# Optimization experiments

Hardware: AMD Instinct MI355X
Metric: run time of the kernel (lower is better)

The kernel has to match this reference:

```python
import jax, jax.numpy as jnp
import numpy as np

K_POW = 3.0
EPS = 1e-6

def _weight1(d, r):
    # (1 - (d/r)^2)^k for d < r else 0; guard base before float power
    base = jnp.where(d < r, 1.0 - (d / r) ** 2, 0.0)
    return base ** K_POW

def _weight2(d, r):
    # 1 for d < r/2; (1 - ((2d-r)/r)^2)^k for r/2 <= d < r; else 0
    band = (d >= r / 2) & (d < r)
    base = jnp.where(band, 1.0 - ((2.0 * d - r) / r) ** 2, 0.0)
    return jnp.where(d < r / 2, 1.0, base ** K_POW)

def setup_inputs() -> dict:
    key = jax.random.key(0)
    ks = jax.random.split(key, 10)
    n, p, L = 4096, 128, 32
    x = jax.random.uniform(ks[0], (n, p), dtype=jnp.float32)
    s = 0.05
    return {
        "x": x,
        "r0": jnp.float32(4.0),
        "r1": jnp.float32(2.0),
        "r2": jnp.float32(4.0),
        "We1": jax.random.normal(ks[1], (L, p), jnp.float32) * s,
        "be1": jnp.zeros((L,), jnp.float32),
        "We2": jax.random.normal(ks[2], (L, L), jnp.float32) * s,
        "be2": jnp.zeros((L,), jnp.float32),
        "Wd1": jax.random.normal(ks[3], (L, L), jnp.float32) * s,
        "bd1": jnp.zeros((L,), jnp.float32),
        "Wd2": jax.random.normal(ks[4], (p, L), jnp.float32) * s,
        "bd2": jnp.zeros((p,), jnp.float32),
    }

def _mr_layer(x, r0, r1, r2):
    y = x  # y = x.clone()
    x2 = jnp.sum(x * x, axis=-1)
    d2 = x2[:, None] + x2[None, :] - 2.0 * (x @ x.T)  # (n, n)
    dist = jnp.sqrt(jnp.maximum(d2, 1e-12))
    md = dist.max()
    # torch reassigns r to max_dist when r > max_dist -> min(r, max_dist)
    r0e = jnp.minimum(r0, md)
    r1e = jnp.minimum(r1, md)
    r2e = jnp.minimum(r2, md)
    # inds = any(dist <= r0) is all-true (diag is ~0), so no row selection needed
    alpha = _weight1(dist, r0e)
    alpha = alpha / jnp.sum(alpha, axis=0, keepdims=True)
    mu = alpha.T @ x  # (n, p)
    mu = jnp.where(jnp.isnan(mu), y, mu)
    U = y - mu  # (n, p); contraction direction per point
    # projection scalar ps[i,j] = <x_i - y_j, U_j>, avoiding (n,n,p) diff tensor
    ps = x @ U.T - jnp.sum(y * U, axis=-1)[None, :]  # (n, n)
    u_norm2 = jnp.sum(U * U, axis=-1)[None, :]  # (1, n)
    dist_u2 = jnp.maximum(ps ** 2 * u_norm2, EPS)
    dist_v = jnp.sqrt(jnp.maximum(dist ** 2 - dist_u2, EPS))
    dist_u = jnp.sqrt(dist_u2)
    beta = _weight2(dist_v, r1e) * _weight2(dist_u, r2e)
    beta = beta / jnp.sum(beta, axis=0, keepdims=True)
    e_Z = beta.T @ x
    e_Z = jnp.where(jnp.isnan(e_Z), y, e_Z)
    return e_Z

def reference(x, r0, r1, r2, We1, be1, We2, be2, Wd1, bd1, Wd2, bd2):
    y = _mr_layer(x, r0, r1, r2)
    # encoder: Linear -> GELU(exact) -> Linear
    h = jax.nn.gelu(y @ We1.T + be1, approximate=False)
    z = h @ We2.T + be2
    # decoder: Linear -> GELU(exact) -> Linear -> Sigmoid
    h2 = jax.nn.gelu(z @ Wd1.T + bd1, approximate=False)
    x_hat = jax.nn.sigmoid(h2 @ Wd2.T + bd2)
    # loss = lam_recon * MSE(x, x_hat); lam_topo = lam_geom = 0
    return jnp.mean((x - x_hat) ** 2)
```

## Files before the change

kernel.cpp:

```cpp
#include <hip/hip_runtime.h>
#include <math.h>

#define N 4096
#define P 128
#define LDIM 32
#define CHUNKS 8
#define ITILES 4

typedef unsigned int u32;
typedef unsigned short u16;
typedef short s16x8 __attribute__((ext_vector_type(8)));
typedef float f32x4 __attribute__((ext_vector_type(4)));

__device__ __forceinline__ u16 f2b(float f) {
  u32 u = __float_as_uint(f);
  u += 0x7fffu + ((u >> 16) & 1u);
  return (u16)(u >> 16);
}
__device__ __forceinline__ float b2f(u16 h) { return __uint_as_float(((u32)h) << 16); }

__device__ __forceinline__ float w2f(float d, float r) {
  if (d < 0.5f * r) return 1.0f;
  if (d < r) { float t = (2.0f * d - r) / r; float b = 1.0f - t * t; return b * b * b; }
  return 0.0f;
}
__device__ __forceinline__ float geluf(float a) {
  return 0.5f * a * (1.0f + erff(a * 0.70710678118654752f));
}

#define MFMA(a, b, c) __builtin_amdgcn_mfma_f32_16x16x32_bf16((a), (b), (c), 0, 0, 0)

__global__ void k_init(u32* __restrict__ mdb, float* __restrict__ out) {
  if (threadIdx.x == 0) { *mdb = 0u; out[0] = 0.0f; }
}

__global__ __launch_bounds__(256) void k_prep(const float* __restrict__ x, u16* __restrict__ xb,
                                              u16* __restrict__ xbT, float* __restrict__ x2) {
  __shared__ u16 tlT[128][40];
  const int bi = blockIdx.x * 32;
  const int tid = threadIdx.x;
  const int r = tid >> 3, cg = (tid & 7) * 16;
  const float* src = &x[(size_t)(bi + r) * P + cg];
  float4 v0 = *(const float4*)(src + 0);
  float4 v1 = *(const float4*)(src + 4);
  float4 v2 = *(const float4*)(src + 8);
  float4 v3 = *(const float4*)(src + 12);
  u16 h[16];
  h[0] = f2b(v0.x); h[1] = f2b(v0.y); h[2] = f2b(v0.z); h[3] = f2b(v0.w);
  h[4] = f2b(v1.x); h[5] = f2b(v1.y); h[6] = f2b(v1.z); h[7] = f2b(v1.w);
  h[8] = f2b(v2.x); h[9] = f2b(v2.y); h[10] = f2b(v2.z); h[11] = f2b(v2.w);
  h[12] = f2b(v3.x); h[13] = f2b(v3.y); h[14] = f2b(v3.z); h[15] = f2b(v3.w);
  float s = 0.0f;
#pragma unroll
  for (int e = 0; e < 16; e++) { float f = b2f(h[e]); s = fmaf(f, f, s); }
  s += __shfl_down(s, 4); s += __shfl_down(s, 2); s += __shfl_down(s, 1);
  if ((tid & 7) == 0) x2[bi + r] = s;
  uint4 p0, p1;
  p0.x = (u32)h[0] | ((u32)h[1] << 16);  p0.y = (u32)h[2] | ((u32)h[3] << 16);
  p0.z = (u32)h[4] | ((u32)h[5] << 16);  p0.w = (u32)h[6] | ((u32)h[7] << 16);
  p1.x = (u32)h[8] | ((u32)h[9] << 16);  p1.y = (u32)h[10] | ((u32)h[11] << 16);
  p1.z = (u32)h[12] | ((u32)h[13] << 16); p1.w = (u32)h[14] | ((u32)h[15] << 16);
  *(uint4*)&xb[(size_t)(bi + r) * P + cg] = p0;
  *(uint4*)&xb[(size_t)(bi + r) * P + cg + 8] = p1;
#pragma unroll
  for (int e = 0; e < 16; e++) tlT[cg + e][r] = h[e];
  __syncthreads();
  const int c = tid >> 1, hh = tid & 1;
  uint4 q0 = *(const uint4*)&tlT[c][hh * 16];
  uint4 q1 = *(const uint4*)&tlT[c][hh * 16 + 8];
  *(uint4*)&xbT[(size_t)c * N + bi + hh * 16] = q0;
  *(uint4*)&xbT[(size_t)c * N + bi + hh * 16 + 8] = q1;
}

__global__ __launch_bounds__(128) void k_anchor(const u16* __restrict__ xb, const float* __restrict__ x2,
                                                u32* __restrict__ mdb) {
  const int i = blockIdx.x * 128 + threadIdx.x;
  const uint4* ra = (const uint4*)(xb + (size_t)i * P);
  const uint4* r0 = (const uint4*)xb;
  float dot = 0.0f;
#pragma unroll
  for (int q = 0; q < 16; ++q) {
    uint4 a = ra[q], b = r0[q];
    u32 aa[4] = {a.x, a.y, a.z, a.w}, bb[4] = {b.x, b.y, b.z, b.w};
#pragma unroll
    for (int e = 0; e < 4; e++) {
      dot = fmaf(b2f((u16)(aa[e] & 0xffffu)), b2f((u16)(bb[e] & 0xffffu)), dot);
      dot = fmaf(b2f((u16)(aa[e] >> 16)), b2f((u16)(bb[e] >> 16)), dot);
    }
  }
  float d2 = fmaxf(x2[i] + x2[0] - 2.0f * dot, 0.0f);
#pragma unroll
  for (int o = 32; o > 0; o >>= 1) d2 = fmaxf(d2, __shfl_down(d2, o));
  if ((threadIdx.x & 63) == 0) atomicMax(mdb, __float_as_uint(d2));
}

__global__ __launch_bounds__(512, 4) void k_grammax(const u16* __restrict__ xb, const float* __restrict__ x2,
                                                    u32* __restrict__ mdb,
                                                    const float* __restrict__ r0p, const float* __restrict__ r1p,
                                                    const float* __restrict__ r2p) {
  const float rmax = fmaxf(r0p[0], fmaxf(r1p[0], r2p[0])) * 1.02f;
  if (__uint_as_float(*mdb) >= rmax * rmax) return;
  __shared__ uint4 LA[1024];
  const int j0 = blockIdx.x * 64;
  const int cid = blockIdx.y;
  if (cid * 512 + 512 <= j0) return;
  const int tid = threadIdx.x;
  const int lane = tid & 63, w = tid >> 6;
  const int lm = lane & 15, quad = lane >> 4;
  {
    const uint4* g = (const uint4*)(xb + (size_t)j0 * P);
#pragma unroll
    for (int it = 0; it < 2; ++it) {
      int c = it * 512 + tid;
      int row = c >> 4, ch = c & 15;
      LA[row * 16 + (ch ^ (row & 7))] = g[c];
    }
  }
  float x2j[4][4];
#pragma unroll
  for (int u = 0; u < 4; u++)
#pragma unroll
    for (int reg = 0; reg < 4; reg++) x2j[u][reg] = x2[j0 + u * 16 + quad * 4 + reg];
  __syncthreads();
  float lmax = 0.0f;
  for (int t = 0; t < ITILES; ++t) {
    const int i0 = cid * 512 + t * 128;
    if (i0 + 128 <= j0) continue;
    f32x4 accG[4];
#pragma unroll
    for (int u = 0; u < 4; u++) accG[u] = {0.f, 0.f, 0.f, 0.f};
    const u16* gb = xb + (size_t)(i0 + w * 16 + lm) * P;
#pragma unroll
    for (int ks = 0; ks < 4; ++ks) {
      s16x8 bf = *(const s16x8*)(gb + ks * 32 + quad * 8);
      s16x8 af[4];
#pragma unroll
      for (int u = 0; u < 4; u++) { int m = u * 16 + lm; af[u] = *(const s16x8*)&LA[m * 16 + ((ks * 4 + quad) ^ (m & 7))]; }
#pragma unroll
      for (int u = 0; u < 4; u++) accG[u] = MFMA(af[u], bf, accG[u]);
    }
    float x2i = x2[i0 + w * 16 + lm];
#pragma unroll
    for (int u = 0; u < 4; u++)
#pragma unroll
      for (int reg = 0; reg < 4; reg++) lmax = fmaxf(lmax, x2j[u][reg] + x2i - 2.0f * accG[u][reg]);
  }
#pragma unroll
  for (int o = 32; o > 0; o >>= 1) lmax = fmaxf(lmax, __shfl_down(lmax, o));
  if (lane == 0) atomicMax(mdb, __float_as_uint(lmax));
}

__global__ __launch_bounds__(512, 4) void k_alpha(const u16* __restrict__ xb, const u16* __restrict__ xbT,
                                                  const float* __restrict__ x2,
                                                  float* __restrict__ muP, float* __restrict__ S1P,
                                                  const float* __restrict__ r0p, const u32* __restrict__ mdb) {
  __shared__ uint4 LA[1024];
  __shared__ u16 W16[64 * 136];
  const int j0 = blockIdx.x * 64, cid = blockIdx.y;
  const int tid = threadIdx.x;
  const int lane = tid & 63, w = tid >> 6;
  const int lm = lane & 15, quad = lane >> 4;
  {
    const uint4* g = (const uint4*)(xb + (size_t)j0 * P);
#pragma unroll
    for (int it = 0; it < 2; ++it) {
      int c = it * 512 + tid;
      int row = c >> 4, ch = c & 15;
      LA[row * 16 + (ch ^ (row & 7))] = g[c];
    }
  }
  const float mdf = sqrtf(fmaxf(__uint_as_float(*mdb), 1e-12f));
  const float re = fminf(r0p[0], mdf);
  const float re2 = re * re, inv_re2 = 1.0f / re2;
  float x2j[4];
#pragma unroll
  for (int v = 0; v < 4; v++) x2j[v] = x2[j0 + v * 16 + lm];
  f32x4 accPV[4], accS[4];
#pragma unroll
  for (int u = 0; u < 4; u++) { accPV[u] = {0.f, 0.f, 0.f, 0.f}; accS[u] = {0.f, 0.f, 0.f, 0.f}; }
  const s16x8 ones = {0x3F80, 0x3F80, 0x3F80, 0x3F80, 0x3F80, 0x3F80, 0x3F80, 0x3F80};
  __syncthreads();
  for (int t = 0; t < ITILES; ++t) {
    const int i0 = cid * 512 + t * 128;
    f32x4 accG[4];
#pragma unroll
    for (int v = 0; v < 4; v++) accG[v] = {0.f, 0.f, 0.f, 0.f};
    const u16* ga = xb + (size_t)(i0 + w * 16 + lm) * P;
#pragma unroll
    for (int ks = 0; ks < 4; ++ks) {
      s16x8 af = *(const s16x8*)(ga + ks * 32 + quad * 8);
      s16x8 bf[4];
#pragma unroll
      for (int v = 0; v < 4; v++) { int m = v * 16 + lm; bf[v] = *(const s16x8*)&LA[m * 16 + ((ks * 4 + quad) ^ (m & 7))]; }
#pragma unroll
      for (int v = 0; v < 4; v++) accG[v] = MFMA(af, bf[v], accG[v]);
    }
    float4 x2iv = *(const float4*)&x2[i0 + w * 16 + quad * 4];
    const float xi[4] = {x2iv.x, x2iv.y, x2iv.z, x2iv.w};
    u16 wv4[4][4];
#pragma unroll
    for (int v = 0; v < 4; v++)
#pragma unroll
      for (int reg = 0; reg < 4; reg++) {
        float d2 = fmaxf(xi[reg] + x2j[v] - 2.0f * accG[v][reg], 1e-12f);
        float wt = 0.0f;
        if (d2 < re2) { float b = 1.0f - d2 * inv_re2; wt = b * b * b; }
        wv4[v][reg] = f2b(wt);
      }
    __syncthreads();
#pragma unroll
    for (int v = 0; v < 4; v++) {
      ushort4 pk; pk.x = wv4[v][0]; pk.y = wv4[v][1]; pk.z = wv4[v][2]; pk.w = wv4[v][3];
      *(ushort4*)&W16[(v * 16 + lm) * 136 + w * 16 + quad * 4] = pk;
    }
    __syncthreads();
    const u16* gx = xbT + (size_t)(w * 16 + lm) * N + i0;
#pragma unroll
    for (int ks = 0; ks < 4; ++ks) {
      s16x8 bx = *(const s16x8*)(gx + ks * 32 + quad * 8);
      s16x8 aw[4];
#pragma unroll
      for (int u = 0; u < 4; u++) { int m = u * 16 + lm; aw[u] = *(const s16x8*)&W16[m * 136 + ks * 32 + quad * 8]; }
#pragma unroll
      for (int u = 0; u < 4; u++) accPV[u] = MFMA(aw[u], bx, accPV[u]);
      if (w == 0) {
#pragma unroll
        for (int u = 0; u < 4; u++) accS[u] = MFMA(aw[u], ones, accS[u]);
      }
    }
  }
  float* mu = muP + (size_t)cid * N * P;
#pragma unroll
  for (int u = 0; u < 4; u++)
#pragma unroll
    for (int reg = 0; reg < 4; reg++)
      mu[(size_t)(j0 + u * 16 + quad * 4 + reg) * P + w * 16 + lm] = accPV[u][reg];
  if (w == 0 && lm == 0) {
#pragma unroll
    for (int u = 0; u < 4; u++)
#pragma unroll
      for (int reg = 0; reg < 4; reg++)
        S1P[cid * N + j0 + u * 16 + quad * 4 + reg] = accS[u][reg];
  }
}

__global__ __launch_bounds__(128) void k_finU(const float* __restrict__ x, const u16* __restrict__ xb,
                                              const float* __restrict__ muP, const float* __restrict__ S1P,
                                              u16* __restrict__ Ub, float* __restrict__ u2, float* __restrict__ cj) {
  const int j = blockIdx.x, t = threadIdx.x;
  float ssum = 0.0f, msum = 0.0f;
#pragma unroll
  for (int c = 0; c < CHUNKS; ++c) {
    ssum += S1P[c * N + j];
    msum += muP[((size_t)c * N + j) * P + t];
  }
  float xv = x[(size_t)j * P + t];
  float uval = 0.0f;
  if (ssum > 0.0f) uval = xv - msum / ssum;
  u16 ub = f2b(uval);
  Ub[(size_t)j * P + t] = ub;
  float uf = b2f(ub);
  float xbf = b2f(xb[(size_t)j * P + t]);
  float a = uf * uf, b = xbf * uf;
#pragma unroll
  for (int o = 32; o > 0; o >>= 1) { a += __shfl_down(a, o); b += __shfl_down(b, o); }
  __shared__ float ra[2], rb[2];
  if ((t & 63) == 0) { ra[t >> 6] = a; rb[t >> 6] = b; }
  __syncthreads();
  if (t == 0) { u2[j] = ra[0] + ra[1]; cj[j] = rb[0] + rb[1]; }
}

__global__ __launch_bounds__(512, 4) void k_betaez(const u16* __restrict__ xb, const u16* __restrict__ Ub,
                                                   const u16* __restrict__ xbT,
                                                   const float* __restrict__ x2, const float* __restrict__ u2,
                                                   const float* __restrict__ cj,
                                                   float* __restrict__ ezP, float* __restrict__ S2P,
                                                   const float* __restrict__ r1p, const float* __restrict__ r2p,
                                                   const u32* __restrict__ mdb) {
  __shared__ uint4 LA[1024];
  __shared__ uint4 LU[1024];
  __shared__ u16 W16[64 * 136];
  const int j0 = blockIdx.x * 64, cid = blockIdx.y;
  const int tid = threadIdx.x;
  const int lane = tid & 63, w = tid >> 6;
  const int lm = lane & 15, quad = lane >> 4;
  {
    const uint4* ga = (const uint4*)(xb + (size_t)j0 * P);
    const uint4* gu = (const uint4*)(Ub + (size_t)j0 * P);
#pragma unroll
    for (int it = 0; it < 2; ++it) {
      int c = it * 512 + tid;
      int row = c >> 4, ch = c & 15;
      int sw = row * 16 + (ch ^ (row & 7));
      LA[sw] = ga[c];
      LU[sw] = gu[c];
    }
  }
  const float mdf = sqrtf(fmaxf(__uint_as_float(*mdb), 1e-12f));
  const float r1e = fminf(r1p[0], mdf), r2e = fminf(r2p[0], mdf);
  float x2j[4], u2j[4], ncj[4];
#pragma unroll
  for (int v = 0; v < 4; v++) {
    int jj = j0 + v * 16 + lm;
    x2j[v] = x2[jj]; u2j[v] = u2[jj]; ncj[v] = -cj[jj];
  }
  f32x4 accPV[4], accS[4];
#pragma unroll
  for (int u = 0; u < 4; u++) { accPV[u] = {0.f, 0.f, 0.f, 0.f}; accS[u] = {0.f, 0.f, 0.f, 0.f}; }
  const s16x8 ones = {0x3F80, 0x3F80, 0x3F80, 0x3F80, 0x3F80, 0x3F80, 0x3F80, 0x3F80};
  __syncthreads();
  for (int t = 0; t < ITILES; ++t) {
    const int i0 = cid * 512 + t * 128;
    f32x4 accG[4], accP[4];
#pragma unroll
    for (int v = 0; v < 4; v++) {
      accG[v] = {0.f, 0.f, 0.f, 0.f};
      accP[v] = {ncj[v], ncj[v], ncj[v], ncj[v]};
    }
    const u16* ga = xb + (size_t)(i0 + w * 16 + lm) * P;
#pragma unroll
    for (int ks = 0; ks < 4; ++ks) {
      s16x8 af = *(const s16x8*)(ga + ks * 32 + quad * 8);
      s16x8 bf[4], bu[4];
#pragma unroll
      for (int v = 0; v < 4; v++) {
        int m = v * 16 + lm;
        int off = m * 16 + ((ks * 4 + quad) ^ (m & 7));
        bf[v] = *(const s16x8*)&LA[off];
        bu[v] = *(const s16x8*)&LU[off];
      }
#pragma unroll
      for (int v = 0; v < 4; v++) {
        accG[v] = MFMA(af, bf[v], accG[v]);
        accP[v] = MFMA(af, bu[v], accP[v]);
      }
    }
    float4 x2iv = *(const float4*)&x2[i0 + w * 16 + quad * 4];
    const float xi[4] = {x2iv.x, x2iv.y, x2iv.z, x2iv.w};
    u16 wv4[4][4];
#pragma unroll
    for (int v = 0; v < 4; v++)
#pragma unroll
      for (int reg = 0; reg < 4; reg++) {
        float d2 = fmaxf(xi[reg] + x2j[v] - 2.0f * accG[v][reg], 1e-12f);
        float ps = accP[v][reg];
        float du2 = fmaxf(ps * ps * u2j[v], 1e-6f);
        float dv = sqrtf(fmaxf(d2 - du2, 1e-6f));
        float du = sqrtf(du2);
        wv4[v][reg] = f2b(w2f(dv, r1e) * w2f(du, r2e));
      }
    __syncthreads();
#pragma unroll
    for (int v = 0; v < 4; v++) {
      ushort4 pk; pk.x = wv4[v][0]; pk.y = wv4[v][1]; pk.z = wv4[v][2]; pk.w = wv4[v][3];
      *(ushort4*)&W16[(v * 16 + lm) * 136 + w * 16 + quad * 4] = pk;
    }
    __syncthreads();
    const u16* gx = xbT + (size_t)(w * 16 + lm) * N + i0;
#pragma unroll
    for (int ks = 0; ks < 4; ++ks) {
      s16x8 bx = *(const s16x8*)(gx + ks * 32 + quad * 8);
      s16x8 aw[4];
#pragma unroll
      for (int u = 0; u < 4; u++) { int m = u * 16 + lm; aw[u] = *(const s16x8*)&W16[m * 136 + ks * 32 + quad * 8]; }
#pragma unroll
      for (int u = 0; u < 4; u++) accPV[u] = MFMA(aw[u], bx, accPV[u]);
      if (w == 0) {
#pragma unroll
        for (int u = 0; u < 4; u++) accS[u] = MFMA(aw[u], ones, accS[u]);
      }
    }
  }
  float* ez = ezP + (size_t)cid * N * P;
#pragma unroll
  for (int u = 0; u < 4; u++)
#pragma unroll
    for (int reg = 0; reg < 4; reg++)
      ez[(size_t)(j0 + u * 16 + quad * 4 + reg) * P + w * 16 + lm] = accPV[u][reg];
  if (w == 0 && lm == 0) {
#pragma unroll
    for (int u = 0; u < 4; u++)
#pragma unroll
      for (int reg = 0; reg < 4; reg++)
        S2P[cid * N + j0 + u * 16 + quad * 4 + reg] = accS[u][reg];
  }
}

#define AE_ROWS 16
__global__ __launch_bounds__(256) void k_ae(const float* __restrict__ x, const float* __restrict__ ezP,
                                            const float* __restrict__ S2P,
                                            const float* __restrict__ We1, const float* __restrict__ be1,
                                            const float* __restrict__ We2, const float* __restrict__ be2,
                                            const float* __restrict__ Wd1, const float* __restrict__ bd1,
                                            const float* __restrict__ Wd2, const float* __restrict__ bd2,
                                            float* __restrict__ out) {
  __shared__ float We1T[P][33];
  __shared__ float We2T[LDIM][33];
  __shared__ float Wd1T[LDIM][33];
  __shared__ float Wd2T[LDIM][129];
  __shared__ float ezs[AE_ROWS][P];
  __shared__ float h1s[AE_ROWS][LDIM], zbs[AE_ROWS][LDIM], h2s[AE_ROWS][LDIM];
  __shared__ float be1s[LDIM], be2s[LDIM], bd1s[LDIM], bd2s[P];
  __shared__ float s2s[AE_ROWS];
  const int tid = threadIdx.x;
  const int r0 = blockIdx.x * AE_ROWS;
  for (int idx = tid; idx < P * LDIM; idx += 256) {
    int o = idx >> 7, k = idx & 127;
    We1T[k][o] = We1[idx];
    int o2 = idx >> 5, k2 = idx & 31;
    Wd2T[k2][o2] = Wd2[idx];
  }
  for (int idx = tid; idx < LDIM * LDIM; idx += 256) {
    int o = idx >> 5, k = idx & 31;
    We2T[k][o] = We2[idx];
    Wd1T[k][o] = Wd1[idx];
  }
  if (tid < LDIM) { be1s[tid] = be1[tid]; be2s[tid] = be2[tid]; bd1s[tid] = bd1[tid]; }
  if (tid < P) bd2s[tid] = bd2[tid];
  if (tid < AE_ROWS) {
    float s = 0.0f;
#pragma unroll
    for (int c = 0; c < CHUNKS; ++c) s += S2P[c * N + r0 + tid];
    s2s[tid] = s;
  }
  __syncthreads();
  for (int idx = tid; idx < AE_ROWS * P; idx += 256) {
    int r = idx >> 7, col = idx & 127;
    int row = r0 + r;
    float es = 0.0f;
#pragma unroll
    for (int c = 0; c < CHUNKS; ++c) es += ezP[((size_t)c * N + row) * P + col];
    float xv = x[(size_t)row * P + col];
    ezs[r][col] = (s2s[r] > 0.0f) ? (es / s2s[r]) : xv;
  }
  __syncthreads();
  {
    const int o = tid & 31, rh = tid >> 5;
#pragma unroll
    for (int rr = 0; rr < 2; rr++) {
      int r = rh + rr * 8;
      float a = be1s[o];
#pragma unroll 8
      for (int k = 0; k < P; k++) a = fmaf(We1T[k][o], ezs[r][k], a);
      h1s[r][o] = geluf(a);
    }
  }
  __syncthreads();
  {
    const int o = tid & 31, rh = tid >> 5;
#pragma unroll
    for (int rr = 0; rr < 2; rr++) {
      int r = rh + rr * 8;
      float a = be2s[o];
#pragma unroll
      for (int k = 0; k < LDIM; k++) a = fmaf(We2T[k][o], h1s[r][k], a);
      zbs[r][o] = a;
    }
  }
  __syncthreads();
  {
    const int o = tid & 31, rh = tid >> 5;
#pragma unroll
    for (int rr = 0; rr < 2; rr++) {
      int r = rh + rr * 8;
      float a = bd1s[o];
#pragma unroll
      for (int k = 0; k < LDIM; k++) a = fmaf(Wd1T[k][o], zbs[r][k], a);
      h2s[r][o] = geluf(a);
    }
  }
  __syncthreads();
  {
    const int o = tid & 127, rh = tid >> 7;
    float part = 0.0f;
#pragma unroll
    for (int rr = 0; rr < 8; rr++) {
      int r = rh + rr * 2;
      int row = r0 + r;
      float a = bd2s[o];
#pragma unroll
      for (int k = 0; k < LDIM; k++) a = fmaf(Wd2T[k][o], h2s[r][k], a);
      float xh = 1.0f / (1.0f + expf(-a));
      float diff = x[(size_t)row * P + o] - xh;
      part = fmaf(diff, diff, part);
    }
#pragma unroll
    for (int off = 32; off > 0; off >>= 1) part += __shfl_down(part, off);
    if ((tid & 63) == 0) atomicAdd(out, part * (1.0f / ((float)N * (float)P)));
  }
}

extern "C" void kernel_launch(void* const* d_in, const int* in_sizes, int n_in,
                              void* d_out, int out_size, void* d_ws, size_t ws_size,
                              hipStream_t stream) {
  const float* x   = (const float*)d_in[0];
  const float* r0  = (const float*)d_in[1];
  const float* r1  = (const float*)d_in[2];
  const float* r2  = (const float*)d_in[3];
  const float* We1 = (const float*)d_in[4];
  const float* be1 = (const float*)d_in[5];
  const float* We2 = (const float*)d_in[6];
  const float* be2 = (const float*)d_in[7];
  const float* Wd1 = (const float*)d_in[8];
  const float* bd1 = (const float*)d_in[9];
  const float* Wd2 = (const float*)d_in[10];
  const float* bd2 = (const float*)d_in[11];
  float* out = (float*)d_out;

  char* base = (char*)d_ws;
  size_t off = 0;
  u16* xb  = (u16*)(base + off); off += (size_t)N * P * 2;
  u16* xbT = (u16*)(base + off); off += (size_t)N * P * 2;
  u16* Ub  = (u16*)(base + off); off += (size_t)N * P * 2;
  float* muP = (float*)(base + off); off += (size_t)CHUNKS * N * P * 4;
  float* ezP = (float*)(base + off); off += (size_t)CHUNKS * N * 4 * P / 4 * 4;
  float* S1P = (float*)(base + off); off += (size_t)CHUNKS * N * 4;
  float* S2P = (float*)(base + off); off += (size_t)CHUNKS * N * 4;
  float* x2  = (float*)(base + off); off += (size_t)N * 4;
  u32* mdb   = (u32*)(base + off); off += 4;
  float* u2  = (float*)(base + off); off += (size_t)N * 4;
  float* cjv = (float*)(base + off); off += (size_t)N * 4;

  hipLaunchKernelGGL(k_init, dim3(1), dim3(64), 0, stream, mdb, out);
  hipLaunchKernelGGL(k_prep, dim3(N / 32), dim3(256), 0, stream, x, xb, xbT, x2);
  hipLaunchKernelGGL(k_anchor, dim3(N / 128), dim3(128), 0, stream, xb, x2, mdb);
  hipLaunchKernelGGL(k_grammax, dim3(N / 64, CHUNKS), dim3(512), 0, stream, xb, x2, mdb, r0, r1, r2);
  hipLaunchKernelGGL(k_alpha, dim3(N / 64, CHUNKS), dim3(512), 0, stream, xb, xbT, x2, muP, S1P, r0, mdb);
  hipLaunchKernelGGL(k_finU, dim3(N), dim3(128), 0, stream, x, xb, muP, S1P, Ub, u2, cjv);
  hipLaunchKernelGGL(k_betaez, dim3(N / 64, CHUNKS), dim3(512), 0, stream, xb, Ub, xbT, x2, u2, cjv, ezP, S2P, r1, r2, mdb);
  hipLaunchKernelGGL(k_ae, dim3(N / AE_ROWS), dim3(256), 0, stream, x, ezP, S2P, We1, be1, We2, be2, Wd1, bd1, Wd2, bd2, out);
}
```

Baseline: 186.9 us.

## Split alpha/beta passes into more chunks, swizzle weight LDS, compute row sums in VALU

Raises the number of i-chunks in the alpha kernel from 8 to 16 and in the beta kernel from 8 to 12 (uneven 3/2 tile split), giving more blocks and higher launch-bound occupancy. The weight tile in LDS switches from a padded layout to an XOR-swizzled layout. The column-sum of weights is now accumulated in registers and reduced through shared-memory atomics, replacing the extra MFMA-against-ones done by wave 0. In exchange, partial buffers grow and the finalize and autoencoder kernels must read more chunks.

```diff
diff --git a/kernel.cpp b/kernel.cpp
--- a/kernel.cpp
+++ b/kernel.cpp
@@ -4,8 +4,8 @@
 #define N 4096
 #define P 128
 #define LDIM 32
-#define CHUNKS 8
-#define ITILES 4
+#define CHA 16
+#define CHB 12
 
 typedef unsigned int u32;
 typedef unsigned short u16;
@@ -123,7 +123,7 @@
     for (int reg = 0; reg < 4; reg++) x2j[u][reg] = x2[j0 + u * 16 + quad * 4 + reg];
   __syncthreads();
   float lmax = 0.0f;
-  for (int t = 0; t < ITILES; ++t) {
+  for (int t = 0; t < 4; ++t) {
     const int i0 = cid * 512 + t * 128;
     if (i0 + 128 <= j0) continue;
     f32x4 accG[4];
@@ -150,12 +150,14 @@
   if (lane == 0) atomicMax(mdb, __float_as_uint(lmax));
 }
 
-__global__ __launch_bounds__(512, 4) void k_alpha(const u16* __restrict__ xb, const u16* __restrict__ xbT,
+__global__ __launch_bounds__(512, 8) void k_alpha(const u16* __restrict__ xb, const u16* __restrict__ xbT,
                                                   const float* __restrict__ x2,
                                                   float* __restrict__ muP, float* __restrict__ S1P,
                                                   const float* __restrict__ r0p, const u32* __restrict__ mdb) {
   __shared__ uint4 LA[1024];
-  __shared__ u16 W16[64 * 136];
+  __shared__ uint4 WS[1024];
+  __shared__ float S1L[64];
+  u16* W16 = (u16*)WS;
   const int j0 = blockIdx.x * 64, cid = blockIdx.y;
   const int tid = threadIdx.x;
   const int lane = tid & 63, w = tid >> 6;
@@ -169,19 +171,21 @@
       LA[row * 16 + (ch ^ (row & 7))] = g[c];
     }
   }
+  if (tid < 64) S1L[tid] = 0.0f;
   const float mdf = sqrtf(fmaxf(__uint_as_float(*mdb), 1e-12f));
   const float re = fminf(r0p[0], mdf);
   const float re2 = re * re, inv_re2 = 1.0f / re2;
   float x2j[4];
 #pragma unroll
   for (int v = 0; v < 4; v++) x2j[v] = x2[j0 + v * 16 + lm];
-  f32x4 accPV[4], accS[4];
-#pragma unroll
-  for (int u = 0; u < 4; u++) { accPV[u] = {0.f, 0.f, 0.f, 0.f}; accS[u] = {0.f, 0.f, 0.f, 0.f}; }
-  const s16x8 ones = {0x3F80, 0x3F80, 0x3F80, 0x3F80, 0x3F80, 0x3F80, 0x3F80, 0x3F80};
-  __syncthreads();
-  for (int t = 0; t < ITILES; ++t) {
-    const int i0 = cid * 512 + t * 128;
+  f32x4 accPV[4];
+#pragma unroll
+  for (int u = 0; u < 4; u++) accPV[u] = {0.f, 0.f, 0.f, 0.f};
+  float sjv[4] = {0.f, 0.f, 0.f, 0.f};
+  __syncthreads();
+#pragma unroll
+  for (int t = 0; t < 2; ++t) {
+    const int i0 = (cid * 2 + t) * 128;
     f32x4 accG[4];
 #pragma unroll
     for (int v = 0; v < 4; v++) accG[v] = {0.f, 0.f, 0.f, 0.f};
@@ -205,13 +209,19 @@
         float d2 = fmaxf(xi[reg] + x2j[v] - 2.0f * accG[v][reg], 1e-12f);
         float wt = 0.0f;
         if (d2 < re2) { float b = 1.0f - d2 * inv_re2; wt = b * b * b; }
-        wv4[v][reg] = f2b(wt);
+        u16 hv = f2b(wt);
+        wv4[v][reg] = hv;
+        sjv[v] += b2f(hv);
       }
     __syncthreads();
-#pragma unroll
-    for (int v = 0; v < 4; v++) {
-      ushort4 pk; pk.x = wv4[v][0]; pk.y = wv4[v][1]; pk.z = wv4[v][2]; pk.w = wv4[v][3];
-      *(ushort4*)&W16[(v * 16 + lm) * 136 + w * 16 + quad * 4] = pk;
+    {
+      const int ch = 2 * w + (quad >> 1), sub = (quad & 1) * 4;
+#pragma unroll
+      for (int v = 0; v < 4; v++) {
+        int row = v * 16 + lm;
+        ushort4 pk; pk.x = wv4[v][0]; pk.y = wv4[v][1]; pk.z = wv4[v][2]; pk.w = wv4[v][3];
+        *(ushort4*)&W16[(row * 16 + (ch ^ (row & 7))) * 8 + sub] = pk;
+      }
     }
     __syncthreads();
     const u16* gx = xbT + (size_t)(w * 16 + lm) * N + i0;
@@ -220,13 +230,12 @@
       s16x8 bx = *(const s16x8*)(gx + ks * 32 + quad * 8);
       s16x8 aw[4];
 #pragma unroll
-      for (int u = 0; u < 4; u++) { int m = u * 16 + lm; aw[u] = *(const s16x8*)&W16[m * 136 + ks * 32 + quad * 8]; }
+      for (int u = 0; u < 4; u++) {
+        int m = u * 16 + lm;
+        aw[u] = *(const s16x8*)&W16[(m * 16 + ((ks * 4 + quad) ^ (m & 7))) * 8];
+      }
 #pragma unroll
       for (int u = 0; u < 4; u++) accPV[u] = MFMA(aw[u], bx, accPV[u]);
-      if (w == 0) {
-#pragma unroll
-        for (int u = 0; u < 4; u++) accS[u] = MFMA(aw[u], ones, accS[u]);
-      }
     }
   }
   float* mu = muP + (size_t)cid * N * P;
@@ -235,13 +244,10 @@
 #pragma unroll
     for (int reg = 0; reg < 4; reg++)
       mu[(size_t)(j0 + u * 16 + quad * 4 + reg) * P + w * 16 + lm] = accPV[u][reg];
-  if (w == 0 && lm == 0) {
-#pragma unroll
-    for (int u = 0; u < 4; u++)
-#pragma unroll
-      for (int reg = 0; reg < 4; reg++)
-        S1P[cid * N + j0 + u * 16 + quad * 4 + reg] = accS[u][reg];
-  }
+#pragma unroll
+  for (int v = 0; v < 4; v++) atomicAdd(&S1L[v * 16 + lm], sjv[v]);
+  __syncthreads();
+  if (tid < 64) S1P[cid * N + j0 + tid] = S1L[tid];
 }
 
 __global__ __launch_bounds__(128) void k_finU(const float* __restrict__ x, const u16* __restrict__ xb,
@@ -250,7 +256,7 @@
   const int j = blockIdx.x, t = threadIdx.x;
   float ssum = 0.0f, msum = 0.0f;
 #pragma unroll
-  for (int c = 0; c < CHUNKS; ++c) {
+  for (int c = 0; c < CHA; ++c) {
     ssum += S1P[c * N + j];
     msum += muP[((size_t)c * N + j) * P + t];
   }
@@ -270,7 +276,7 @@
   if (t == 0) { u2[j] = ra[0] + ra[1]; cj[j] = rb[0] + rb[1]; }
 }
 
-__global__ __launch_bounds__(512, 4) void k_betaez(const u16* __restrict__ xb, const u16* __restrict__ Ub,
+__global__ __launch_bounds__(512, 6) void k_betaez(const u16* __restrict__ xb, const u16* __restrict__ Ub,
                                                    const u16* __restrict__ xbT,
                                                    const float* __restrict__ x2, const float* __restrict__ u2,
                                                    const float* __restrict__ cj,
@@ -279,7 +285,9 @@
                                                    const u32* __restrict__ mdb) {
   __shared__ uint4 LA[1024];
   __shared__ uint4 LU[1024];
-  __shared__ u16 W16[64 * 136];
+  __shared__ uint4 WS[1024];
+  __shared__ float S2L[64];
+  u16* W16 = (u16*)WS;
   const int j0 = blockIdx.x * 64, cid = blockIdx.y;
   const int tid = threadIdx.x;
   const int lane = tid & 63, w = tid >> 6;
@@ -296,6 +304,7 @@
       LU[sw] = gu[c];
     }
   }
+  if (tid < 64) S2L[tid] = 0.0f;
   const float mdf = sqrtf(fmaxf(__uint_as_float(*mdb), 1e-12f));
   const float r1e = fminf(r1p[0], mdf), r2e = fminf(r2p[0], mdf);
   float x2j[4], u2j[4], ncj[4];
@@ -304,13 +313,15 @@
     int jj = j0 + v * 16 + lm;
     x2j[v] = x2[jj]; u2j[v] = u2[jj]; ncj[v] = -cj[jj];
   }
-  f32x4 accPV[4], accS[4];
-#pragma unroll
-  for (int u = 0; u < 4; u++) { accPV[u] = {0.f, 0.f, 0.f, 0.f}; accS[u] = {0.f, 0.f, 0.f, 0.f}; }
-  const s16x8 ones = {0x3F80, 0x3F80, 0x3F80, 0x3F80, 0x3F80, 0x3F80, 0x3F80, 0x3F80};
-  __syncthreads();
-  for (int t = 0; t < ITILES; ++t) {
-    const int i0 = cid * 512 + t * 128;
+  f32x4 accPV[4];
+#pragma unroll
+  for (int u = 0; u < 4; u++) accPV[u] = {0.f, 0.f, 0.f, 0.f};
+  float sjv[4] = {0.f, 0.f, 0.f, 0.f};
+  const int tstart = (cid < 8) ? cid * 3 : 24 + (cid - 8) * 2;
+  const int tcnt = (cid < 8) ? 3 : 2;
+  __syncthreads();
+  for (int t = 0; t < tcnt; ++t) {
+    const int i0 = (tstart + t) * 128;
     f32x4 accG[4], accP[4];
 #pragma unroll
     for (int v = 0; v < 4; v++) {
@@ -347,13 +358,19 @@
         float du2 = fmaxf(ps * ps * u2j[v], 1e-6f);
         float dv = sqrtf(fmaxf(d2 - du2, 1e-6f));
         float du = sqrtf(du2);
-        wv4[v][reg] = f2b(w2f(dv, r1e) * w2f(du, r2e));
+        u16 hv = f2b(w2f(dv, r1e) * w2f(du, r2e));
+        wv4[v][reg] = hv;
+        sjv[v] += b2f(hv);
       }
     __syncthreads();
-#pragma unroll
-    for (int v = 0; v < 4; v++) {
-      ushort4 pk; pk.x = wv4[v][0]; pk.y = wv4[v][1]; pk.z = wv4[v][2]; pk.w = wv4[v][3];
-      *(ushort4*)&W16[(v * 16 + lm) * 136 + w * 16 + quad * 4] = pk;
+    {
+      const int ch = 2 * w + (quad >> 1), sub = (quad & 1) * 4;
+#pragma unroll
+      for (int v = 0; v < 4; v++) {
+        int row = v * 16 + lm;
+        ushort4 pk; pk.x = wv4[v][0]; pk.y = wv4[v][1]; pk.z = wv4[v][2]; pk.w = wv4[v][3];
+        *(ushort4*)&W16[(row * 16 + (ch ^ (row & 7))) * 8 + sub] = pk;
+      }
     }
     __syncthreads();
     const u16* gx = xbT + (size_t)(w * 16 + lm) * N + i0;
@@ -362,13 +379,12 @@
       s16x8 bx = *(const s16x8*)(gx + ks * 32 + quad * 8);
       s16x8 aw[4];
 #pragma unroll
-      for (int u = 0; u < 4; u++) { int m = u * 16 + lm; aw[u] = *(const s16x8*)&W16[m * 136 + ks * 32 + quad * 8]; }
+      for (int u = 0; u < 4; u++) {
+        int m = u * 16 + lm;
+        aw[u] = *(const s16x8*)&W16[(m * 16 + ((ks * 4 + quad) ^ (m & 7))) * 8];
+      }
 #pragma unroll
       for (int u = 0; u < 4; u++) accPV[u] = MFMA(aw[u], bx, accPV[u]);
-      if (w == 0) {
-#pragma unroll
-        for (int u = 0; u < 4; u++) accS[u] = MFMA(aw[u], ones, accS[u]);
-      }
     }
   }
   float* ez = ezP + (size_t)cid * N * P;
@@ -377,13 +393,10 @@
 #pragma unroll
     for (int reg = 0; reg < 4; reg++)
       ez[(size_t)(j0 + u * 16 + quad * 4 + reg) * P + w * 16 + lm] = accPV[u][reg];
-  if (w == 0 && lm == 0) {
-#pragma unroll
-    for (int u = 0; u < 4; u++)
-#pragma unroll
-      for (int reg = 0; reg < 4; reg++)
-        S2P[cid * N + j0 + u * 16 + quad * 4 + reg] = accS[u][reg];
-  }
+#pragma unroll
+  for (int v = 0; v < 4; v++) atomicAdd(&S2L[v * 16 + lm], sjv[v]);
+  __syncthreads();
+  if (tid < 64) S2P[cid * N + j0 + tid] = S2L[tid];
 }
 
 #define AE_ROWS 16
@@ -420,7 +433,7 @@
   if (tid < AE_ROWS) {
     float s = 0.0f;
 #pragma unroll
-    for (int c = 0; c < CHUNKS; ++c) s += S2P[c * N + r0 + tid];
+    for (int c = 0; c < CHB; ++c) s += S2P[c * N + r0 + tid];
     s2s[tid] = s;
   }
   __syncthreads();
@@ -429,7 +442,7 @@
     int row = r0 + r;
     float es = 0.0f;
 #pragma unroll
-    for (int c = 0; c < CHUNKS; ++c) es += ezP[((size_t)c * N + row) * P + col];
+    for (int c = 0; c < CHB; ++c) es += ezP[((size_t)c * N + row) * P + col];
     float xv = x[(size_t)row * P + col];
     ezs[r][col] = (s2s[r] > 0.0f) ? (es / s2s[r]) : xv;
   }
@@ -512,10 +525,10 @@
   u16* xb  = (u16*)(base + off); off += (size_t)N * P * 2;
   u16* xbT = (u16*)(base + off); off += (size_t)N * P * 2;
   u16* Ub  = (u16*)(base + off); off += (size_t)N * P * 2;
-  float* muP = (float*)(base + off); off += (size_t)CHUNKS * N * P * 4;
-  float* ezP = (float*)(base + off); off += (size_t)CHUNKS * N * 4 * P / 4 * 4;
-  float* S1P = (float*)(base + off); off += (size_t)CHUNKS * N * 4;
-  float* S2P = (float*)(base + off); off += (size_t)CHUNKS * N * 4;
+  float* muP = (float*)(base + off); off += (size_t)CHA * N * P * 4;
+  float* ezP = (float*)(base + off); off += (size_t)CHB * N * P * 4;
+  float* S1P = (float*)(base + off); off += (size_t)CHA * N * 4;
+  float* S2P = (float*)(base + off); off += (size_t)CHB * N * 4;
   float* x2  = (float*)(base + off); off += (size_t)N * 4;
   u32* mdb   = (u32*)(base + off); off += 4;
   float* u2  = (float*)(base + off); off += (size_t)N * 4;
@@ -524,9 +537,9 @@
   hipLaunchKernelGGL(k_init, dim3(1), dim3(64), 0, stream, mdb, out);
   hipLaunchKernelGGL(k_prep, dim3(N / 32), dim3(256), 0, stream, x, xb, xbT, x2);
   hipLaunchKernelGGL(k_anchor, dim3(N / 128), dim3(128), 0, stream, xb, x2, mdb);
-  hipLaunchKernelGGL(k_grammax, dim3(N / 64, CHUNKS), dim3(512), 0, stream, xb, x2, mdb, r0, r1, r2);
-  hipLaunchKernelGGL(k_alpha, dim3(N / 64, CHUNKS), dim3(512), 0, stream, xb, xbT, x2, muP, S1P, r0, mdb);
+  hipLaunchKernelGGL(k_grammax, dim3(N / 64, 8), dim3(512), 0, stream, xb, x2, mdb, r0, r1, r2);
+  hipLaunchKernelGGL(k_alpha, dim3(N / 64, CHA), dim3(512), 0, stream, xb, xbT, x2, muP, S1P, r0, mdb);
   hipLaunchKernelGGL(k_finU, dim3(N), dim3(128), 0, stream, x, xb, muP, S1P, Ub, u2, cjv);
-  hipLaunchKernelGGL(k_betaez, dim3(N / 64, CHUNKS), dim3(512), 0, stream, xb, Ub, xbT, x2, u2, cjv, ezP, S2P, r1, r2, mdb);
+  hipLaunchKernelGGL(k_betaez, dim3(N / 64, CHB), dim3(512), 0, stream, xb, Ub, xbT, x2, u2, cjv, ezP, S2P, r1, r2, mdb);
   hipLaunchKernelGGL(k_ae, dim3(N / AE_ROWS), dim3(256), 0, stream, x, ezP, S2P, We1, be1, We2, be2, Wd1, bd1, Wd2, bd2, out);
 }
```

Result: slower. 228.8 us (+22.4%).
